# Performance work log

Hardware: AMD Instinct MI355X
Metric: run time of the kernel (lower is better)

The kernel has to match this reference:

```python
import jax, jax.numpy as jnp
import numpy as np

B, N, DIN = 2, 4096, 128
DQK, DV, H = 128, 128, 8
DH = DQK // H  # head dim for q/k
DVH = DV // H  # head dim for v


def setup_inputs() -> dict:
    key = jax.random.key(0)
    ks = jax.random.split(key, 6)
    x = jax.random.normal(ks[0], (B, N, DIN), dtype=jnp.float32)
    # node mask: first batch fully valid, second batch padded to 3/4 length
    lengths = jnp.array([N, 3 * N // 4])
    mask = jnp.arange(N)[None, :] < lengths[:, None]  # [B, N] bool
    # fused q|k|non_att projection (dim_qk*2 + dim_in outputs)
    W1 = jax.random.normal(ks[1], (DIN, DQK * 2 + DIN), dtype=jnp.float32) * (DIN ** -0.5)
    b1 = jnp.zeros((DQK * 2 + DIN,), dtype=jnp.float32)
    Wv = jax.random.normal(ks[2], (DIN, DV), dtype=jnp.float32) * (DIN ** -0.5)
    bv = jnp.zeros((DV,), dtype=jnp.float32)
    Wo = jax.random.normal(ks[3], (DV, DIN), dtype=jnp.float32) * (DV ** -0.5)
    bo = jnp.zeros((DIN,), dtype=jnp.float32)
    return {"x": x, "mask": mask, "W1": W1, "b1": b1, "Wv": Wv, "bv": bv, "Wo": Wo, "bo": bo}


def reference(x, mask, W1, b1, Wv, bv, Wo, bo):
    # x: [B,N,DIN], mask: [B,N] bool (True = valid node)
    m = mask[..., None].astype(x.dtype)  # [B,N,1]
    # fc_1: fused [q | k | non_att], masked like batch_like(..., skip_masking=False)
    h = (x @ W1 + b1) * m  # [B,N,2*DQK+DIN]
    q = h[..., :DQK]
    k = h[..., DQK:2 * DQK]
    non_att = h[..., -DIN:]
    # fc_v, masked
    v = (x @ Wv + bv) * m  # [B,N,DV]
    # multi-head attention coefficients (AttnCoef(1,1)): masked softmax over keys
    qh = q.reshape(B, N, H, DH)
    kh = k.reshape(B, N, H, DH)
    scores = jnp.einsum('bqhd,bkhd->bhqk', qh, kh) / (DH ** 0.5)  # [B,H,N,N]
    neg = jnp.asarray(jnp.finfo(scores.dtype).min, scores.dtype)
    scores = jnp.where(mask[:, None, None, :], scores, neg)
    alpha = jax.nn.softmax(scores, axis=-1)  # [B,H,N,N]
    # apply_attn: per-head weighted sum of v
    vh = v.reshape(B, N, H, DVH)
    att = jnp.einsum('bhqk,bkhd->bqhd', alpha, vh).reshape(B, N, DV)
    # fc_o (dropout p=0 -> identity), masked; add_batch residual with non_att
    out = (att @ Wo + bo) * m
    return (non_att + out) * m
```

## Files before the change

kernel.cpp:

```cpp
#include <hip/hip_runtime.h>
#include <hip/hip_fp16.h>
#include <math.h>

#define BATCH 2
#define SEQ   4096
#define DIN   128
#define NH    8
#define DHD   16
#define MROWS (BATCH * SEQ)
#define QSCALE 0.36067376022224085f

typedef _Float16 h4 __attribute__((ext_vector_type(4)));
typedef _Float16 h8 __attribute__((ext_vector_type(8)));
typedef float    f4 __attribute__((ext_vector_type(4)));

typedef union { h8 v; unsigned u[4]; } H8U;

__device__ __forceinline__ int keyperm(int k) {
    return ((k >> 5) & 1) * 32 + ((k >> 2) & 3) * 8 + ((k >> 4) & 1) * 4 + (k & 3);
}

__global__ __launch_bounds__(512) void proj_kernel(
    const float* __restrict__ x, const int* __restrict__ mask,
    const float* __restrict__ W1, const float* __restrict__ Wv,
    const float* __restrict__ b1, const float* __restrict__ bv,
    _Float16* __restrict__ qT, _Float16* __restrict__ kT,
    _Float16* __restrict__ vT4, _Float16* __restrict__ natT)
{
    __shared__ __align__(16) char SMEM[128 * 136 * 2];
    _Float16* Tw  = (_Float16*)SMEM;
    _Float16* T16 = (_Float16*)SMEM;

    const int t = threadIdx.x;
    const int w = t >> 6, lane = t & 63, quad = lane >> 4, mr = lane & 15;
    const int flat   = blockIdx.x + 4 * blockIdx.y;
    const int region = flat >> 6;
    const int row0   = (flat & 63) * 128;
    const int col0   = region * 128;

    if (mask[row0] == 0) return;

    const float* wsrc = (region < 3) ? (W1 + col0) : Wv;
    const int wstride = (region < 3) ? 384 : 128;
    float4 wv[8];
#pragma unroll
    for (int i = 0; i < 8; ++i) {
        int idx = t + i * 512;
        int k = idx >> 5, c4 = idx & 31;
        wv[i] = *reinterpret_cast<const float4*>(wsrc + (size_t)k * wstride + c4 * 4);
    }
    float4 xv[8];
    {
        const float* xrow = x + (size_t)(row0 + w * 16 + mr) * 128;
#pragma unroll
        for (int ks = 0; ks < 4; ++ks) {
            xv[2 * ks]     = *reinterpret_cast<const float4*>(xrow + ks * 32 + quad * 8);
            xv[2 * ks + 1] = *reinterpret_cast<const float4*>(xrow + ks * 32 + quad * 8 + 4);
        }
    }

#pragma unroll
    for (int i = 0; i < 8; ++i) {
        int idx = t + i * 512;
        int k = idx >> 5, c4 = idx & 31;
        Tw[(c4 * 4 + 0) * 136 + k] = (_Float16)wv[i].x;
        Tw[(c4 * 4 + 1) * 136 + k] = (_Float16)wv[i].y;
        Tw[(c4 * 4 + 2) * 136 + k] = (_Float16)wv[i].z;
        Tw[(c4 * 4 + 3) * 136 + k] = (_Float16)wv[i].w;
    }
    h8 a[4];
#pragma unroll
    for (int ks = 0; ks < 4; ++ks) {
        h8 av;
        av[0] = (_Float16)xv[2*ks].x;   av[1] = (_Float16)xv[2*ks].y;
        av[2] = (_Float16)xv[2*ks].z;   av[3] = (_Float16)xv[2*ks].w;
        av[4] = (_Float16)xv[2*ks+1].x; av[5] = (_Float16)xv[2*ks+1].y;
        av[6] = (_Float16)xv[2*ks+1].z; av[7] = (_Float16)xv[2*ks+1].w;
        a[ks] = av;
    }
    __syncthreads();

    f4 acc[8];
#pragma unroll
    for (int ct = 0; ct < 8; ++ct) {
        f4 ac = {0.f, 0.f, 0.f, 0.f};
#pragma unroll
        for (int ks = 0; ks < 4; ++ks) {
            h8 bb = *reinterpret_cast<const h8*>(
                &Tw[(ct * 16 + mr) * 136 + ks * 32 + quad * 8]);
            ac = __builtin_amdgcn_mfma_f32_16x16x32_f16(a[ks], bb, ac, 0, 0, 0);
        }
        acc[ct] = ac;
    }
    __syncthreads();

    if (region <= 1) {
        float scale = (region == 0) ? QSCALE : 1.0f;
#pragma unroll
        for (int ct = 0; ct < 8; ++ct) {
            float bias = b1[col0 + ct * 16 + mr];
#pragma unroll
            for (int reg = 0; reg < 4; ++reg) {
                int lr = w * 16 + quad * 4 + reg;
                T16[lr * 136 + ct * 16 + mr] =
                    (_Float16)((acc[ct][reg] + bias) * scale);
            }
        }
        __syncthreads();
        _Float16* dstbase = (region == 0) ? qT : kT;
#pragma unroll
        for (int i = 0; i < 4; ++i) {
            int idx = t + i * 512;
            int h = idx >> 8, rr = (idx >> 1) & 127, half = idx & 1;
            *reinterpret_cast<h8*>(
                dstbase + ((size_t)h * MROWS + row0 + rr) * 16 + half * 8) =
                *reinterpret_cast<h8*>(&T16[rr * 136 + h * 16 + half * 8]);
        }
    } else if (region == 2) {
#pragma unroll
        for (int ct = 0; ct < 8; ++ct) {
            float bias = b1[256 + ct * 16 + mr];
#pragma unroll
            for (int reg = 0; reg < 4; ++reg) {
                int m = w * 16 + quad * 4 + reg;
                T16[(ct * 16 + mr) * 136 + m] = (_Float16)(acc[ct][reg] + bias);
            }
        }
        __syncthreads();
#pragma unroll
        for (int i = 0; i < 4; ++i) {
            int idx = t + i * 512;
            int c = idx >> 4, seg = idx & 15;
            *reinterpret_cast<h8*>(natT + (size_t)c * MROWS + row0 + seg * 8) =
                *reinterpret_cast<h8*>(&T16[c * 136 + seg * 8]);
        }
    } else {
#pragma unroll
        for (int ct = 0; ct < 8; ++ct) {
            float bias = bv[ct * 16 + mr];
#pragma unroll
            for (int reg = 0; reg < 4; ++reg) {
                int m = w * 16 + quad * 4 + reg;
                int sub = m >> 6, ml = m & 63;
                T16[(ct * 16 + mr) * 136 + sub * 64 + keyperm(ml)] =
                    (_Float16)(acc[ct][reg] + bias);
            }
        }
        __syncthreads();
#pragma unroll
        for (int i = 0; i < 4; ++i) {
            int idx = t + i * 512;
            int c = idx >> 4, sub = (idx >> 3) & 1, seg = idx & 7;
            int h = c >> 4, d = c & 15;
            int tile = (flat & 63) * 2 + sub;
            *reinterpret_cast<h8*>(
                vT4 + ((size_t)(h * 128 + tile) * 16 + d) * 64 + seg * 8) =
                *reinterpret_cast<h8*>(&T16[c * 136 + sub * 64 + seg * 8]);
        }
    }
}

#define LOADT(K0, K1, K2, K3, V0, V1, TILE)                                   \
    do {                                                                      \
        const _Float16* kp_ = kbase + (size_t)(TILE) * 1024;                  \
        const _Float16* vp_ = vbase + (size_t)(TILE) * 1024;                  \
        K0 = *reinterpret_cast<const h4*>(kp_);                               \
        K1 = *reinterpret_cast<const h4*>(kp_ + 256);                         \
        K2 = *reinterpret_cast<const h4*>(kp_ + 512);                         \
        K3 = *reinterpret_cast<const h4*>(kp_ + 768);                         \
        V0 = *reinterpret_cast<const h8*>(vp_);                               \
        V1 = *reinterpret_cast<const h8*>(vp_ + 32);                         \
    } while (0)

#define PROC_SUB(AQ, K0, K1, K2, K3, V0, V1, O, L)                            \
    do {                                                                      \
        f4 st0 = __builtin_amdgcn_mfma_f32_16x16x16f16(K0, AQ, fzero, 0, 0, 0); \
        f4 st1 = __builtin_amdgcn_mfma_f32_16x16x16f16(K1, AQ, fzero, 0, 0, 0); \
        f4 st2 = __builtin_amdgcn_mfma_f32_16x16x16f16(K2, AQ, fzero, 0, 0, 0); \
        f4 st3 = __builtin_amdgcn_mfma_f32_16x16x16f16(K3, AQ, fzero, 0, 0, 0); \
        H8U pa, pb;                                                           \
        pa.u[0] = __builtin_bit_cast(unsigned, __builtin_amdgcn_cvt_pkrtz(    \
            __builtin_amdgcn_exp2f(st0[0]), __builtin_amdgcn_exp2f(st0[1]))); \
        pa.u[1] = __builtin_bit_cast(unsigned, __builtin_amdgcn_cvt_pkrtz(    \
            __builtin_amdgcn_exp2f(st0[2]), __builtin_amdgcn_exp2f(st0[3]))); \
        pa.u[2] = __builtin_bit_cast(unsigned, __builtin_amdgcn_cvt_pkrtz(    \
            __builtin_amdgcn_exp2f(st1[0]), __builtin_amdgcn_exp2f(st1[1]))); \
        pa.u[3] = __builtin_bit_cast(unsigned, __builtin_amdgcn_cvt_pkrtz(    \
            __builtin_amdgcn_exp2f(st1[2]), __builtin_amdgcn_exp2f(st1[3]))); \
        pb.u[0] = __builtin_bit_cast(unsigned, __builtin_amdgcn_cvt_pkrtz(    \
            __builtin_amdgcn_exp2f(st2[0]), __builtin_amdgcn_exp2f(st2[1]))); \
        pb.u[1] = __builtin_bit_cast(unsigned, __builtin_amdgcn_cvt_pkrtz(    \
            __builtin_amdgcn_exp2f(st2[2]), __builtin_amdgcn_exp2f(st2[3]))); \
        pb.u[2] = __builtin_bit_cast(unsigned, __builtin_amdgcn_cvt_pkrtz(    \
            __builtin_amdgcn_exp2f(st3[0]), __builtin_amdgcn_exp2f(st3[1]))); \
        pb.u[3] = __builtin_bit_cast(unsigned, __builtin_amdgcn_cvt_pkrtz(    \
            __builtin_amdgcn_exp2f(st3[2]), __builtin_amdgcn_exp2f(st3[3]))); \
        O = __builtin_amdgcn_mfma_f32_16x16x32_f16(pa.v, V0, O, 0, 0, 0);     \
        L = __builtin_amdgcn_mfma_f32_16x16x32_f16(pa.v, vones, L, 0, 0, 0);  \
        O = __builtin_amdgcn_mfma_f32_16x16x32_f16(pb.v, V1, O, 0, 0, 0);     \
        L = __builtin_amdgcn_mfma_f32_16x16x32_f16(pb.v, vones, L, 0, 0, 0);  \
    } while (0)

#define COMBINE(OC, LC, CIDX)                                                 \
    do {                                                                      \
        _Pragma("unroll")                                                     \
        for (int reg = 0; reg < 4; ++reg) {                                   \
            float of = OC[reg] + Cmb[0][wq][lane][(CIDX)*4 + reg]             \
                               + Cmb[1][wq][lane][(CIDX)*4 + reg]             \
                               + Cmb[2][wq][lane][(CIDX)*4 + reg];            \
            float lf = LC[reg] + Cmb[0][wq][lane][16 + (CIDX)*4 + reg]        \
                               + Cmb[1][wq][lane][16 + (CIDX)*4 + reg]        \
                               + Cmb[2][wq][lane][16 + (CIDX)*4 + reg];       \
            att16[(size_t)(m0 + (CIDX)*16 + quad * 4 + reg) * 128             \
                  + hh * DHD + mr] = (_Float16)(of / lf);                     \
        }                                                                     \
    } while (0)

__global__ __launch_bounds__(512) void attn_kernel(
    const _Float16* __restrict__ qT, const _Float16* __restrict__ kT,
    const _Float16* __restrict__ vT4, const int* __restrict__ mask,
    _Float16* __restrict__ att16)
{
    __shared__ float Cmb[3][2][64][33];

    const int flat = blockIdx.x + 32 * blockIdx.y + 256 * blockIdx.z;
    const int hh = flat & 7;
    const int qt = (flat >> 3) & 31;
    const int b  = flat >> 8;

    const int t = threadIdx.x;
    const int w = t >> 6, lane = t & 63, quad = lane >> 4, mr = lane & 15;
    const int wq = w & 1;
    const int g  = w >> 1;
    const int m0 = b * SEQ + qt * 128 + wq * 64;

    if (mask[b * SEQ + qt * 128] == 0) return;

    int tv = mask[b * SEQ + lane * 64];
    const int ntiles = (int)__popcll(__ballot(tv != 0));
    const int quarter = ntiles >> 2;
    const int tbeg = g * quarter;
    const int tend = tbeg + quarter;

    const h4 aQ0 = *reinterpret_cast<const h4*>(
        qT + ((size_t)hh * MROWS + m0 + mr) * DHD + quad * 4);
    const h4 aQ1 = *reinterpret_cast<const h4*>(
        qT + ((size_t)hh * MROWS + m0 + 16 + mr) * DHD + quad * 4);
    const h4 aQ2 = *reinterpret_cast<const h4*>(
        qT + ((size_t)hh * MROWS + m0 + 32 + mr) * DHD + quad * 4);
    const h4 aQ3 = *reinterpret_cast<const h4*>(
        qT + ((size_t)hh * MROWS + m0 + 48 + mr) * DHD + quad * 4);

    const _Float16* kbase = kT + ((size_t)hh * MROWS + b * SEQ + mr) * DHD + quad * 4;
    const _Float16* vbase = vT4 + ((size_t)(hh * 128 + b * 64) * 16 + mr) * 64 + quad * 8;

    const f4 fzero = {0.f, 0.f, 0.f, 0.f};
    const _Float16 one = (_Float16)1.0f;
    const h8 vones = {one, one, one, one, one, one, one, one};

    h4 ka0, ka1, ka2, ka3, kb0, kb1, kb2, kb3;
    h8 va0, va1, vb0, vb1;
    LOADT(ka0, ka1, ka2, ka3, va0, va1, tbeg);
    LOADT(kb0, kb1, kb2, kb3, vb0, vb1, tbeg + 1);

    f4 O0 = fzero, O1 = fzero, O2 = fzero, O3 = fzero;
    f4 L0 = fzero, L1 = fzero, L2 = fzero, L3 = fzero;

    for (int it = tbeg; it < tend; it += 2) {
        __builtin_amdgcn_s_setprio(1);
        PROC_SUB(aQ0, ka0, ka1, ka2, ka3, va0, va1, O0, L0);
        PROC_SUB(aQ1, ka0, ka1, ka2, ka3, va0, va1, O1, L1);
        PROC_SUB(aQ2, ka0, ka1, ka2, ka3, va0, va1, O2, L2);
        PROC_SUB(aQ3, ka0, ka1, ka2, ka3, va0, va1, O3, L3);
        __builtin_amdgcn_s_setprio(0);
        int nA = (it + 2 < tend) ? (it + 2) : it;
        LOADT(ka0, ka1, ka2, ka3, va0, va1, nA);

        __builtin_amdgcn_s_setprio(1);
        PROC_SUB(aQ0, kb0, kb1, kb2, kb3, vb0, vb1, O0, L0);
        PROC_SUB(aQ1, kb0, kb1, kb2, kb3, vb0, vb1, O1, L1);
        PROC_SUB(aQ2, kb0, kb1, kb2, kb3, vb0, vb1, O2, L2);
        PROC_SUB(aQ3, kb0, kb1, kb2, kb3, vb0, vb1, O3, L3);
        __builtin_amdgcn_s_setprio(0);
        int nB = (it + 3 < tend) ? (it + 3) : (it + 1);
        LOADT(kb0, kb1, kb2, kb3, vb0, vb1, nB);
    }

    if (g != 0) {
        float* dst = &Cmb[g - 1][wq][lane][0];
#pragma unroll
        for (int reg = 0; reg < 4; ++reg) {
            dst[reg]      = O0[reg];
            dst[4 + reg]  = O1[reg];
            dst[8 + reg]  = O2[reg];
            dst[12 + reg] = O3[reg];
            dst[16 + reg] = L0[reg];
            dst[20 + reg] = L1[reg];
            dst[24 + reg] = L2[reg];
            dst[28 + reg] = L3[reg];
        }
    }
    __syncthreads();
    if (g == 0) {
        COMBINE(O0, L0, 0);
        COMBINE(O1, L1, 1);
        COMBINE(O2, L2, 2);
        COMBINE(O3, L3, 3);
    }
}

__global__ __launch_bounds__(256) void outproj_kernel(
    const _Float16* __restrict__ att16, const float* __restrict__ Wo,
    const _Float16* __restrict__ natT, const int* __restrict__ mask,
    const float* __restrict__ bo, float* __restrict__ out)
{
    __shared__ __align__(16) _Float16 Tw[32 * 136];
    __shared__ __align__(16) float   To[64 * 36];

    const int t = threadIdx.x;
    const int w = t >> 6, lane = t & 63, quad = lane >> 4, mr = lane & 15;
    const int row0 = blockIdx.x * 64;
    const int m0w  = row0 + w * 16;
    const int c0   = blockIdx.y * 32;

    if (mask[row0] == 0) {
#pragma unroll
        for (int i = 0; i < 2; ++i) {
            int idx = t + i * 256;
            int r = idx >> 3, c4 = idx & 7;
            *reinterpret_cast<float4*>(
                out + (size_t)(row0 + r) * 128 + c0 + c4 * 4) =
                (float4){0.f, 0.f, 0.f, 0.f};
        }
        return;
    }

    float4 wv[4];
#pragma unroll
    for (int i = 0; i < 4; ++i) {
        int idx = t + i * 256;
        int k = idx >> 3, c4 = idx & 7;
        wv[i] = *reinterpret_cast<const float4*>(Wo + (size_t)k * 128 + c0 + c4 * 4);
    }
    h8 a[4];
#pragma unroll
    for (int ks = 0; ks < 4; ++ks)
        a[ks] = *reinterpret_cast<const h8*>(
            att16 + (size_t)(m0w + mr) * 128 + ks * 32 + quad * 8);
    h4 nv[2];
#pragma unroll
    for (int ct = 0; ct < 2; ++ct)
        nv[ct] = *reinterpret_cast<const h4*>(
            natT + (size_t)(c0 + ct * 16 + mr) * MROWS + m0w + quad * 4);
#pragma unroll
    for (int i = 0; i < 4; ++i) {
        int idx = t + i * 256;
        int k = idx >> 3, c4 = idx & 7;
        Tw[(c4 * 4 + 0) * 136 + k] = (_Float16)wv[i].x;
        Tw[(c4 * 4 + 1) * 136 + k] = (_Float16)wv[i].y;
        Tw[(c4 * 4 + 2) * 136 + k] = (_Float16)wv[i].z;
        Tw[(c4 * 4 + 3) * 136 + k] = (_Float16)wv[i].w;
    }
    __syncthreads();

    f4 acc[2];
#pragma unroll
    for (int ct = 0; ct < 2; ++ct) {
        f4 ac = {0.f, 0.f, 0.f, 0.f};
#pragma unroll
        for (int ks = 0; ks < 4; ++ks) {
            h8 bb = *reinterpret_cast<const h8*>(
                &Tw[(ct * 16 + mr) * 136 + ks * 32 + quad * 8]);
            ac = __builtin_amdgcn_mfma_f32_16x16x32_f16(a[ks], bb, ac, 0, 0, 0);
        }
        acc[ct] = ac;
    }

#pragma unroll
    for (int ct = 0; ct < 2; ++ct) {
        float bias = bo[c0 + ct * 16 + mr];
#pragma unroll
        for (int reg = 0; reg < 4; ++reg) {
            int lr = w * 16 + quad * 4 + reg;
            To[lr * 36 + ct * 16 + mr] = acc[ct][reg] + bias + (float)nv[ct][reg];
        }
    }
    __syncthreads();
#pragma unroll
    for (int i = 0; i < 2; ++i) {
        int idx = t + i * 256;
        int r = idx >> 3, c4 = idx & 7;
        *reinterpret_cast<float4*>(
            out + (size_t)(row0 + r) * 128 + c0 + c4 * 4) =
            *reinterpret_cast<float4*>(&To[r * 36 + c4 * 4]);
    }
}

extern "C" void kernel_launch(void* const* d_in, const int* in_sizes, int n_in,
                              void* d_out, int out_size, void* d_ws, size_t ws_size,
                              hipStream_t stream) {
    const float* x    = (const float*)d_in[0];
    const int*   mask = (const int*)  d_in[1];
    const float* W1   = (const float*)d_in[2];
    const float* b1   = (const float*)d_in[3];
    const float* Wv   = (const float*)d_in[4];
    const float* bv   = (const float*)d_in[5];
    const float* Wo   = (const float*)d_in[6];
    const float* bo   = (const float*)d_in[7];
    float* out = (float*)d_out;

    _Float16* qT    = (_Float16*)d_ws;
    _Float16* kT    = qT    + (size_t)NH * MROWS * DHD;
    _Float16* vT4   = kT    + (size_t)NH * MROWS * DHD;
    _Float16* att16 = vT4   + (size_t)DIN * MROWS;
    _Float16* natT  = att16 + (size_t)MROWS * DIN;

    proj_kernel<<<dim3(4, MROWS / 128), 512, 0, stream>>>(
        x, mask, W1, Wv, b1, bv, qT, kT, vT4, natT);
    attn_kernel<<<dim3(SEQ / 128, NH, BATCH), 512, 0, stream>>>(
        qT, kT, vT4, mask, att16);
    outproj_kernel<<<dim3(MROWS / 64, 4), 256, 0, stream>>>(
        att16, Wo, natT, mask, bo, out);
}
```

Measured before the change: 110.2 us.

## Fuse output projection into attention kernel via per-head atomic accumulation

Removes the separate output-projection kernel. The projection kernel now writes non_att plus both biases straight into the fp32 output, and zeroes masked rows. Each attention block multiplies its per-head attention slice by the matching 16 rows of Wo with an MFMA and atomically adds the result into the output. This drops one launch and the att16/natT round trips through memory, at the cost of many fp32 atomic adds to each output element and a summation order that is no longer deterministic.

```diff
diff --git a/kernel.cpp b/kernel.cpp
--- a/kernel.cpp
+++ b/kernel.cpp
@@ -24,8 +24,9 @@
     const float* __restrict__ x, const int* __restrict__ mask,
     const float* __restrict__ W1, const float* __restrict__ Wv,
     const float* __restrict__ b1, const float* __restrict__ bv,
+    const float* __restrict__ bo,
     _Float16* __restrict__ qT, _Float16* __restrict__ kT,
-    _Float16* __restrict__ vT4, _Float16* __restrict__ natT)
+    _Float16* __restrict__ vT4, float* __restrict__ out)
 {
     __shared__ __align__(16) char SMEM[128 * 136 * 2];
     _Float16* Tw  = (_Float16*)SMEM;
@@ -38,7 +39,19 @@
     const int row0   = (flat & 63) * 128;
     const int col0   = region * 128;
 
-    if (mask[row0] == 0) return;
+    if (mask[row0] == 0) {
+        if (region == 2) {
+#pragma unroll
+            for (int i = 0; i < 8; ++i) {
+                int idx = t + i * 512;
+                int r = idx >> 5, c4 = idx & 31;
+                *reinterpret_cast<float4*>(
+                    out + (size_t)(row0 + r) * 128 + c4 * 4) =
+                    (float4){0.f, 0.f, 0.f, 0.f};
+            }
+        }
+        return;
+    }
 
     const float* wsrc = (region < 3) ? (W1 + col0) : Wv;
     const int wstride = (region < 3) ? 384 : 128;
@@ -119,20 +132,13 @@
     } else if (region == 2) {
 #pragma unroll
         for (int ct = 0; ct < 8; ++ct) {
-            float bias = b1[256 + ct * 16 + mr];
+            float bias = b1[256 + ct * 16 + mr] + bo[ct * 16 + mr];
 #pragma unroll
             for (int reg = 0; reg < 4; ++reg) {
-                int m = w * 16 + quad * 4 + reg;
-                T16[(ct * 16 + mr) * 136 + m] = (_Float16)(acc[ct][reg] + bias);
+                int lr = w * 16 + quad * 4 + reg;
+                out[(size_t)(row0 + lr) * 128 + ct * 16 + mr] =
+                    acc[ct][reg] + bias;
             }
-        }
-        __syncthreads();
-#pragma unroll
-        for (int i = 0; i < 4; ++i) {
-            int idx = t + i * 512;
-            int c = idx >> 4, seg = idx & 15;
-            *reinterpret_cast<h8*>(natT + (size_t)c * MROWS + row0 + seg * 8) =
-                *reinterpret_cast<h8*>(&T16[c * 136 + seg * 8]);
         }
     } else {
 #pragma unroll
@@ -201,7 +207,7 @@
         L = __builtin_amdgcn_mfma_f32_16x16x32_f16(pb.v, vones, L, 0, 0, 0);  \
     } while (0)
 
-#define COMBINE(OC, LC, CIDX)                                                 \
+#define COMB2(OC, LC, CIDX)                                                   \
     do {                                                                      \
         _Pragma("unroll")                                                     \
         for (int reg = 0; reg < 4; ++reg) {                                   \
@@ -211,17 +217,17 @@
             float lf = LC[reg] + Cmb[0][wq][lane][16 + (CIDX)*4 + reg]        \
                                + Cmb[1][wq][lane][16 + (CIDX)*4 + reg]        \
                                + Cmb[2][wq][lane][16 + (CIDX)*4 + reg];       \
-            att16[(size_t)(m0 + (CIDX)*16 + quad * 4 + reg) * 128             \
-                  + hh * DHD + mr] = (_Float16)(of / lf);                     \
+            av[(CIDX)*4 + reg] = (_Float16)(of / lf);                         \
         }                                                                     \
     } while (0)
 
 __global__ __launch_bounds__(512) void attn_kernel(
     const _Float16* __restrict__ qT, const _Float16* __restrict__ kT,
     const _Float16* __restrict__ vT4, const int* __restrict__ mask,
-    _Float16* __restrict__ att16)
+    const float* __restrict__ Wo, float* __restrict__ out)
 {
     __shared__ float Cmb[3][2][64][33];
+    _Float16* att_s = (_Float16*)Cmb;
 
     const int flat = blockIdx.x + 32 * blockIdx.y + 256 * blockIdx.z;
     const int hh = flat & 7;
@@ -301,98 +307,36 @@
         }
     }
     __syncthreads();
+    _Float16 av[16];
     if (g == 0) {
-        COMBINE(O0, L0, 0);
-        COMBINE(O1, L1, 1);
-        COMBINE(O2, L2, 2);
-        COMBINE(O3, L3, 3);
-    }
-}
-
-__global__ __launch_bounds__(256) void outproj_kernel(
-    const _Float16* __restrict__ att16, const float* __restrict__ Wo,
-    const _Float16* __restrict__ natT, const int* __restrict__ mask,
-    const float* __restrict__ bo, float* __restrict__ out)
-{
-    __shared__ __align__(16) _Float16 Tw[32 * 136];
-    __shared__ __align__(16) float   To[64 * 36];
-
-    const int t = threadIdx.x;
-    const int w = t >> 6, lane = t & 63, quad = lane >> 4, mr = lane & 15;
-    const int row0 = blockIdx.x * 64;
-    const int m0w  = row0 + w * 16;
-    const int c0   = blockIdx.y * 32;
-
-    if (mask[row0] == 0) {
-#pragma unroll
-        for (int i = 0; i < 2; ++i) {
-            int idx = t + i * 256;
-            int r = idx >> 3, c4 = idx & 7;
-            *reinterpret_cast<float4*>(
-                out + (size_t)(row0 + r) * 128 + c0 + c4 * 4) =
-                (float4){0.f, 0.f, 0.f, 0.f};
-        }
-        return;
-    }
-
-    float4 wv[4];
-#pragma unroll
-    for (int i = 0; i < 4; ++i) {
-        int idx = t + i * 256;
-        int k = idx >> 3, c4 = idx & 7;
-        wv[i] = *reinterpret_cast<const float4*>(Wo + (size_t)k * 128 + c0 + c4 * 4);
-    }
-    h8 a[4];
-#pragma unroll
-    for (int ks = 0; ks < 4; ++ks)
-        a[ks] = *reinterpret_cast<const h8*>(
-            att16 + (size_t)(m0w + mr) * 128 + ks * 32 + quad * 8);
-    h4 nv[2];
-#pragma unroll
-    for (int ct = 0; ct < 2; ++ct)
-        nv[ct] = *reinterpret_cast<const h4*>(
-            natT + (size_t)(c0 + ct * 16 + mr) * MROWS + m0w + quad * 4);
-#pragma unroll
-    for (int i = 0; i < 4; ++i) {
-        int idx = t + i * 256;
-        int k = idx >> 3, c4 = idx & 7;
-        Tw[(c4 * 4 + 0) * 136 + k] = (_Float16)wv[i].x;
-        Tw[(c4 * 4 + 1) * 136 + k] = (_Float16)wv[i].y;
-        Tw[(c4 * 4 + 2) * 136 + k] = (_Float16)wv[i].z;
-        Tw[(c4 * 4 + 3) * 136 + k] = (_Float16)wv[i].w;
-    }
-    __syncthreads();
-
-    f4 acc[2];
-#pragma unroll
-    for (int ct = 0; ct < 2; ++ct) {
-        f4 ac = {0.f, 0.f, 0.f, 0.f};
-#pragma unroll
-        for (int ks = 0; ks < 4; ++ks) {
-            h8 bb = *reinterpret_cast<const h8*>(
-                &Tw[(ct * 16 + mr) * 136 + ks * 32 + quad * 8]);
-            ac = __builtin_amdgcn_mfma_f32_16x16x32_f16(a[ks], bb, ac, 0, 0, 0);
-        }
-        acc[ct] = ac;
-    }
-
-#pragma unroll
-    for (int ct = 0; ct < 2; ++ct) {
-        float bias = bo[c0 + ct * 16 + mr];
-#pragma unroll
-        for (int reg = 0; reg < 4; ++reg) {
-            int lr = w * 16 + quad * 4 + reg;
-            To[lr * 36 + ct * 16 + mr] = acc[ct][reg] + bias + (float)nv[ct][reg];
-        }
-    }
-    __syncthreads();
-#pragma unroll
-    for (int i = 0; i < 2; ++i) {
-        int idx = t + i * 256;
-        int r = idx >> 3, c4 = idx & 7;
-        *reinterpret_cast<float4*>(
-            out + (size_t)(row0 + r) * 128 + c0 + c4 * 4) =
-            *reinterpret_cast<float4*>(&To[r * 36 + c4 * 4]);
+        COMB2(O0, L0, 0);
+        COMB2(O1, L1, 1);
+        COMB2(O2, L2, 2);
+        COMB2(O3, L3, 3);
+    }
+    __syncthreads();
+    if (g == 0) {
+#pragma unroll
+        for (int i = 0; i < 16; ++i) {
+            int cidx = i >> 2, reg = i & 3;
+            att_s[(wq * 64 + cidx * 16 + quad * 4 + reg) * 20 + mr] = av[i];
+        }
+    }
+    __syncthreads();
+
+    const h4 aA = *reinterpret_cast<const h4*>(&att_s[(w * 16 + mr) * 20 + quad * 4]);
+    const float* wop = Wo + (size_t)(hh * DHD + quad * 4) * 128 + mr;
+    const size_t orow = (size_t)(b * SEQ + qt * 128 + w * 16 + quad * 4);
+#pragma unroll
+    for (int ct = 0; ct < 8; ++ct) {
+        h4 bB;
+#pragma unroll
+        for (int j = 0; j < 4; ++j)
+            bB[j] = (_Float16)wop[(size_t)j * 128 + ct * 16];
+        f4 oa = __builtin_amdgcn_mfma_f32_16x16x16f16(aA, bB, fzero, 0, 0, 0);
+#pragma unroll
+        for (int reg = 0; reg < 4; ++reg)
+            unsafeAtomicAdd(out + (orow + reg) * 128 + ct * 16 + mr, oa[reg]);
     }
 }
 
@@ -412,13 +356,9 @@
     _Float16* qT    = (_Float16*)d_ws;
     _Float16* kT    = qT    + (size_t)NH * MROWS * DHD;
     _Float16* vT4   = kT    + (size_t)NH * MROWS * DHD;
-    _Float16* att16 = vT4   + (size_t)DIN * MROWS;
-    _Float16* natT  = att16 + (size_t)MROWS * DIN;
 
     proj_kernel<<<dim3(4, MROWS / 128), 512, 0, stream>>>(
-        x, mask, W1, Wv, b1, bv, qT, kT, vT4, natT);
+        x, mask, W1, Wv, b1, bv, bo, qT, kT, vT4, out);
     attn_kernel<<<dim3(SEQ / 128, NH, BATCH), 512, 0, stream>>>(
-        qT, kT, vT4, mask, att16);
-    outproj_kernel<<<dim3(MROWS / 64, 4), 256, 0, stream>>>(
-        att16, Wo, natT, mask, bo, out);
+        qT, kT, vT4, mask, Wo, out);
 }
```

After: 121.6 us. 1.1x slower.

## Fuse residual non_att path into output buffer and accumulate outproj in place

Applied to the files above, without the earlier changes.

The non-attention projection now writes bias-added results directly into the fp32 output, and the output projection adds its result onto out via read-modify-write, removing the fp16 natT intermediate buffer. Projection blocks are halved to 64 rows with waves split across column halves, and outproj uses 16-column tiles. This trades one intermediate buffer round trip for an fp32 read-modify-write of the output and less coalesced scalar stores.

```diff
diff --git a/kernel.cpp b/kernel.cpp
--- a/kernel.cpp
+++ b/kernel.cpp
@@ -24,21 +24,38 @@
     const float* __restrict__ x, const int* __restrict__ mask,
     const float* __restrict__ W1, const float* __restrict__ Wv,
     const float* __restrict__ b1, const float* __restrict__ bv,
+    const float* __restrict__ bo,
     _Float16* __restrict__ qT, _Float16* __restrict__ kT,
-    _Float16* __restrict__ vT4, _Float16* __restrict__ natT)
+    _Float16* __restrict__ vT4, float* __restrict__ out)
 {
     __shared__ __align__(16) char SMEM[128 * 136 * 2];
     _Float16* Tw  = (_Float16*)SMEM;
     _Float16* T16 = (_Float16*)SMEM;
+    _Float16* T16v = (_Float16*)SMEM;
 
     const int t = threadIdx.x;
     const int w = t >> 6, lane = t & 63, quad = lane >> 4, mr = lane & 15;
+    const int rw = w >> 1;
+    const int ch = w & 1;
     const int flat   = blockIdx.x + 4 * blockIdx.y;
-    const int region = flat >> 6;
-    const int row0   = (flat & 63) * 128;
+    const int region = flat >> 7;
+    const int rowblk = flat & 127;
+    const int row0   = rowblk * 64;
     const int col0   = region * 128;
 
-    if (mask[row0] == 0) return;
+    if (mask[row0] == 0) {
+        if (region == 2) {
+#pragma unroll
+            for (int i = 0; i < 4; ++i) {
+                int idx = t + i * 512;
+                int r = idx >> 5, c4 = idx & 31;
+                *reinterpret_cast<float4*>(
+                    out + (size_t)(row0 + r) * 128 + c4 * 4) =
+                    (float4){0.f, 0.f, 0.f, 0.f};
+            }
+        }
+        return;
+    }
 
     const float* wsrc = (region < 3) ? (W1 + col0) : Wv;
     const int wstride = (region < 3) ? 384 : 128;
@@ -51,7 +68,7 @@
     }
     float4 xv[8];
     {
-        const float* xrow = x + (size_t)(row0 + w * 16 + mr) * 128;
+        const float* xrow = x + (size_t)(row0 + rw * 16 + mr) * 128;
 #pragma unroll
         for (int ks = 0; ks < 4; ++ks) {
             xv[2 * ks]     = *reinterpret_cast<const float4*>(xrow + ks * 32 + quad * 8);
@@ -80,82 +97,81 @@
     }
     __syncthreads();
 
-    f4 acc[8];
-#pragma unroll
-    for (int ct = 0; ct < 8; ++ct) {
+    f4 acc[4];
+#pragma unroll
+    for (int ct2 = 0; ct2 < 4; ++ct2) {
+        int c = ch * 4 + ct2;
         f4 ac = {0.f, 0.f, 0.f, 0.f};
 #pragma unroll
         for (int ks = 0; ks < 4; ++ks) {
             h8 bb = *reinterpret_cast<const h8*>(
-                &Tw[(ct * 16 + mr) * 136 + ks * 32 + quad * 8]);
+                &Tw[(c * 16 + mr) * 136 + ks * 32 + quad * 8]);
             ac = __builtin_amdgcn_mfma_f32_16x16x32_f16(a[ks], bb, ac, 0, 0, 0);
         }
-        acc[ct] = ac;
-    }
+        acc[ct2] = ac;
+    }
+
+    if (region == 2) {
+#pragma unroll
+        for (int ct2 = 0; ct2 < 4; ++ct2) {
+            int c = ch * 4 + ct2;
+            float bias = b1[256 + c * 16 + mr] + bo[c * 16 + mr];
+#pragma unroll
+            for (int reg = 0; reg < 4; ++reg) {
+                int lr = rw * 16 + quad * 4 + reg;
+                out[(size_t)(row0 + lr) * 128 + c * 16 + mr] =
+                    acc[ct2][reg] + bias;
+            }
+        }
+        return;
+    }
+
     __syncthreads();
 
     if (region <= 1) {
         float scale = (region == 0) ? QSCALE : 1.0f;
 #pragma unroll
-        for (int ct = 0; ct < 8; ++ct) {
-            float bias = b1[col0 + ct * 16 + mr];
+        for (int ct2 = 0; ct2 < 4; ++ct2) {
+            int c = ch * 4 + ct2;
+            float bias = b1[col0 + c * 16 + mr];
 #pragma unroll
             for (int reg = 0; reg < 4; ++reg) {
-                int lr = w * 16 + quad * 4 + reg;
-                T16[lr * 136 + ct * 16 + mr] =
-                    (_Float16)((acc[ct][reg] + bias) * scale);
+                int lr = rw * 16 + quad * 4 + reg;
+                T16[lr * 136 + c * 16 + mr] =
+                    (_Float16)((acc[ct2][reg] + bias) * scale);
             }
         }
         __syncthreads();
         _Float16* dstbase = (region == 0) ? qT : kT;
 #pragma unroll
-        for (int i = 0; i < 4; ++i) {
+        for (int i = 0; i < 2; ++i) {
             int idx = t + i * 512;
-            int h = idx >> 8, rr = (idx >> 1) & 127, half = idx & 1;
+            int h = idx >> 7, rr = (idx >> 1) & 63, half = idx & 1;
             *reinterpret_cast<h8*>(
                 dstbase + ((size_t)h * MROWS + row0 + rr) * 16 + half * 8) =
                 *reinterpret_cast<h8*>(&T16[rr * 136 + h * 16 + half * 8]);
         }
-    } else if (region == 2) {
-#pragma unroll
-        for (int ct = 0; ct < 8; ++ct) {
-            float bias = b1[256 + ct * 16 + mr];
+    } else {
+#pragma unroll
+        for (int ct2 = 0; ct2 < 4; ++ct2) {
+            int c = ch * 4 + ct2;
+            float bias = bv[c * 16 + mr];
 #pragma unroll
             for (int reg = 0; reg < 4; ++reg) {
-                int m = w * 16 + quad * 4 + reg;
-                T16[(ct * 16 + mr) * 136 + m] = (_Float16)(acc[ct][reg] + bias);
+                int ml = rw * 16 + quad * 4 + reg;
+                T16v[(c * 16 + mr) * 72 + keyperm(ml)] =
+                    (_Float16)(acc[ct2][reg] + bias);
             }
         }
         __syncthreads();
 #pragma unroll
-        for (int i = 0; i < 4; ++i) {
+        for (int i = 0; i < 2; ++i) {
             int idx = t + i * 512;
-            int c = idx >> 4, seg = idx & 15;
-            *reinterpret_cast<h8*>(natT + (size_t)c * MROWS + row0 + seg * 8) =
-                *reinterpret_cast<h8*>(&T16[c * 136 + seg * 8]);
-        }
-    } else {
-#pragma unroll
-        for (int ct = 0; ct < 8; ++ct) {
-            float bias = bv[ct * 16 + mr];
-#pragma unroll
-            for (int reg = 0; reg < 4; ++reg) {
-                int m = w * 16 + quad * 4 + reg;
-                int sub = m >> 6, ml = m & 63;
-                T16[(ct * 16 + mr) * 136 + sub * 64 + keyperm(ml)] =
-                    (_Float16)(acc[ct][reg] + bias);
-            }
-        }
-        __syncthreads();
-#pragma unroll
-        for (int i = 0; i < 4; ++i) {
-            int idx = t + i * 512;
-            int c = idx >> 4, sub = (idx >> 3) & 1, seg = idx & 7;
+            int c = idx >> 3, seg = idx & 7;
             int h = c >> 4, d = c & 15;
-            int tile = (flat & 63) * 2 + sub;
             *reinterpret_cast<h8*>(
-                vT4 + ((size_t)(h * 128 + tile) * 16 + d) * 64 + seg * 8) =
-                *reinterpret_cast<h8*>(&T16[c * 136 + sub * 64 + seg * 8]);
+                vT4 + ((size_t)(h * 128 + rowblk) * 16 + d) * 64 + seg * 8) =
+                *reinterpret_cast<h8*>(&T16v[c * 72 + seg * 8]);
         }
     }
 }
@@ -311,35 +327,23 @@
 
 __global__ __launch_bounds__(256) void outproj_kernel(
     const _Float16* __restrict__ att16, const float* __restrict__ Wo,
-    const _Float16* __restrict__ natT, const int* __restrict__ mask,
-    const float* __restrict__ bo, float* __restrict__ out)
+    const int* __restrict__ mask, float* __restrict__ out)
 {
-    __shared__ __align__(16) _Float16 Tw[32 * 136];
-    __shared__ __align__(16) float   To[64 * 36];
+    __shared__ __align__(16) _Float16 Tw[16 * 136];
 
     const int t = threadIdx.x;
     const int w = t >> 6, lane = t & 63, quad = lane >> 4, mr = lane & 15;
     const int row0 = blockIdx.x * 64;
     const int m0w  = row0 + w * 16;
-    const int c0   = blockIdx.y * 32;
-
-    if (mask[row0] == 0) {
-#pragma unroll
-        for (int i = 0; i < 2; ++i) {
-            int idx = t + i * 256;
-            int r = idx >> 3, c4 = idx & 7;
-            *reinterpret_cast<float4*>(
-                out + (size_t)(row0 + r) * 128 + c0 + c4 * 4) =
-                (float4){0.f, 0.f, 0.f, 0.f};
-        }
-        return;
-    }
-
-    float4 wv[4];
-#pragma unroll
-    for (int i = 0; i < 4; ++i) {
+    const int c0   = blockIdx.y * 16;
+
+    if (mask[row0] == 0) return;
+
+    float4 wv[2];
+#pragma unroll
+    for (int i = 0; i < 2; ++i) {
         int idx = t + i * 256;
-        int k = idx >> 3, c4 = idx & 7;
+        int k = idx >> 2, c4 = idx & 3;
         wv[i] = *reinterpret_cast<const float4*>(Wo + (size_t)k * 128 + c0 + c4 * 4);
     }
     h8 a[4];
@@ -347,15 +351,10 @@
     for (int ks = 0; ks < 4; ++ks)
         a[ks] = *reinterpret_cast<const h8*>(
             att16 + (size_t)(m0w + mr) * 128 + ks * 32 + quad * 8);
-    h4 nv[2];
-#pragma unroll
-    for (int ct = 0; ct < 2; ++ct)
-        nv[ct] = *reinterpret_cast<const h4*>(
-            natT + (size_t)(c0 + ct * 16 + mr) * MROWS + m0w + quad * 4);
-#pragma unroll
-    for (int i = 0; i < 4; ++i) {
+#pragma unroll
+    for (int i = 0; i < 2; ++i) {
         int idx = t + i * 256;
-        int k = idx >> 3, c4 = idx & 7;
+        int k = idx >> 2, c4 = idx & 3;
         Tw[(c4 * 4 + 0) * 136 + k] = (_Float16)wv[i].x;
         Tw[(c4 * 4 + 1) * 136 + k] = (_Float16)wv[i].y;
         Tw[(c4 * 4 + 2) * 136 + k] = (_Float16)wv[i].z;
@@ -363,36 +362,19 @@
     }
     __syncthreads();
 
-    f4 acc[2];
-#pragma unroll
-    for (int ct = 0; ct < 2; ++ct) {
-        f4 ac = {0.f, 0.f, 0.f, 0.f};
-#pragma unroll
-        for (int ks = 0; ks < 4; ++ks) {
-            h8 bb = *reinterpret_cast<const h8*>(
-                &Tw[(ct * 16 + mr) * 136 + ks * 32 + quad * 8]);
-            ac = __builtin_amdgcn_mfma_f32_16x16x32_f16(a[ks], bb, ac, 0, 0, 0);
-        }
-        acc[ct] = ac;
-    }
-
-#pragma unroll
-    for (int ct = 0; ct < 2; ++ct) {
-        float bias = bo[c0 + ct * 16 + mr];
-#pragma unroll
-        for (int reg = 0; reg < 4; ++reg) {
-            int lr = w * 16 + quad * 4 + reg;
-            To[lr * 36 + ct * 16 + mr] = acc[ct][reg] + bias + (float)nv[ct][reg];
-        }
-    }
-    __syncthreads();
-#pragma unroll
-    for (int i = 0; i < 2; ++i) {
-        int idx = t + i * 256;
-        int r = idx >> 3, c4 = idx & 7;
-        *reinterpret_cast<float4*>(
-            out + (size_t)(row0 + r) * 128 + c0 + c4 * 4) =
-            *reinterpret_cast<float4*>(&To[r * 36 + c4 * 4]);
+    f4 ac = {0.f, 0.f, 0.f, 0.f};
+#pragma unroll
+    for (int ks = 0; ks < 4; ++ks) {
+        h8 bb = *reinterpret_cast<const h8*>(
+            &Tw[mr * 136 + ks * 32 + quad * 8]);
+        ac = __builtin_amdgcn_mfma_f32_16x16x32_f16(a[ks], bb, ac, 0, 0, 0);
+    }
+
+#pragma unroll
+    for (int reg = 0; reg < 4; ++reg) {
+        int lr = w * 16 + quad * 4 + reg;
+        size_t idx = (size_t)(row0 + lr) * 128 + c0 + mr;
+        out[idx] = out[idx] + ac[reg];
     }
 }
 
@@ -413,12 +395,11 @@
     _Float16* kT    = qT    + (size_t)NH * MROWS * DHD;
     _Float16* vT4   = kT    + (size_t)NH * MROWS * DHD;
     _Float16* att16 = vT4   + (size_t)DIN * MROWS;
-    _Float16* natT  = att16 + (size_t)MROWS * DIN;
-
-    proj_kernel<<<dim3(4, MROWS / 128), 512, 0, stream>>>(
-        x, mask, W1, Wv, b1, bv, qT, kT, vT4, natT);
+
+    proj_kernel<<<dim3(4, 128), 512, 0, stream>>>(
+        x, mask, W1, Wv, b1, bv, bo, qT, kT, vT4, out);
     attn_kernel<<<dim3(SEQ / 128, NH, BATCH), 512, 0, stream>>>(
         qT, kT, vT4, mask, att16);
-    outproj_kernel<<<dim3(MROWS / 64, 4), 256, 0, stream>>>(
-        att16, Wo, natT, mask, bo, out);
+    outproj_kernel<<<dim3(MROWS / 64, 8), 256, 0, stream>>>(
+        att16, Wo, mask, out);
 }
```

Result: slower. 113.7 us (+3.1%).
